# Performance work log

Hardware: AMD Instinct MI355X
Metric: run time of the kernel (lower is better)

Reference implementation:

```python
import jax, jax.numpy as jnp
import numpy as np

TOP_K = 12
OBS_RADIUS = 1.0
DIST_MIN_THRES = 0.8
EPS = 1e-4


def setup_inputs() -> dict:
    key = jax.random.key(0)
    ks = jax.random.split(key, 9)
    N, in_dim = 4096, 4
    c = in_dim + 2  # pairwise diff + eye flag + (dist - thres)
    states = jax.random.normal(ks[0], (N, in_dim), dtype=jnp.float32) * 2.0
    def w(k, o, i):
        return jax.random.normal(k, (o, i), dtype=jnp.float32) * (1.0 / np.sqrt(i))
    return {
        "states": states,
        "W1": w(ks[1], 64, c),  "b1": jnp.zeros((64,), jnp.float32),
        "W2": w(ks[2], 128, 64), "b2": jnp.zeros((128,), jnp.float32),
        "W3": w(ks[3], 64, 128), "b3": jnp.zeros((64,), jnp.float32),
        "W4": w(ks[4], 1, 64),   "b4": jnp.zeros((1,), jnp.float32),
    }


def _conv1x1(h, W, b):
    # h: [N, C_in, L]; 1x1 Conv1d == channel matmul
    return jnp.einsum('oi,nil->nol', W, h) + b[None, :, None]


def reference(states, W1, b1, W2, b2, W3, b3, W4, b4):
    N = states.shape[0]
    # pairwise differences: [N, N, in_dim]
    x = states[:, None, :] - states[None, :, :]
    d_norm = jnp.sqrt(jnp.sum(jnp.square(x[:, :, :2]) + EPS, axis=2))  # [N, N]
    eye = jnp.eye(N, dtype=x.dtype)
    x = jnp.concatenate(
        [x, eye[:, :, None], (d_norm - DIST_MIN_THRES)[:, :, None]], axis=2
    )  # [N, N, c]
    # remove_distant_agents: keep TOP_K nearest neighbors per agent
    dn = jnp.sqrt(jnp.sum(jnp.square(x[:, :, :2]) + EPS, axis=2))  # [N, N]
    _, idx = jax.lax.top_k(-dn, TOP_K)                              # [N, k]
    x = jnp.take_along_axis(x, idx[:, :, None], axis=1)            # [N, k, c]
    dist = jnp.sqrt(jnp.sum(jnp.square(x[:, :, :2]) + EPS, axis=2, keepdims=True))  # [N,k,1]
    k, c = x.shape[1], x.shape[2]
    mask = (dist <= OBS_RADIUS).astype(x.dtype).reshape(-1, 1, k)  # [N,1,k] (reshape, as in source)
    h = x.reshape(-1, c, k)  # faithful: source uses reshape, NOT transpose
    h = jax.nn.relu(_conv1x1(h, W1, b1))
    h = jax.nn.relu(_conv1x1(h, W2, b2))
    h = jax.nn.relu(_conv1x1(h, W3, b3))
    h = _conv1x1(h, W4, b4)  # [N, 1, k]
    h = h * mask
    return h, mask
```

## Files before the change

kernel.cpp:

```cpp
#include <hip/hip_runtime.h>
#include <stdint.h>

#define NAG 4096
#define TOPK 12
#define EPSF 1e-4f
#define NT 256
#define PT (NAG / NT)
#define MTOT (NAG * TOPK)

typedef unsigned long long u64;
typedef short short8v __attribute__((ext_vector_type(8)));
typedef float f32x4 __attribute__((ext_vector_type(4)));

__device__ __forceinline__ u64 umin64(u64 a, u64 b) { return a < b ? a : b; }

__device__ __forceinline__ unsigned short f2bf(float f) {
    union { float f; unsigned u; } v; v.f = f;
    unsigned r = v.u + 0x7FFFu + ((v.u >> 16) & 1u);
    return (unsigned short)(r >> 16);
}

template <int CTRL>
__device__ __forceinline__ void dpp_min_step(unsigned &hi, unsigned &lo) {
    unsigned ohi = (unsigned)__builtin_amdgcn_update_dpp((int)hi, (int)hi, CTRL, 0xf, 0xf, false);
    unsigned olo = (unsigned)__builtin_amdgcn_update_dpp((int)lo, (int)lo, CTRL, 0xf, 0xf, false);
    bool t = (ohi < hi) || (ohi == hi && olo < lo);
    hi = t ? ohi : hi;
    lo = t ? olo : lo;
}

__global__ __launch_bounds__(NT, 8)
void cbf_select(const float* __restrict__ states,
                float* __restrict__ xbuf,
                float* __restrict__ out)
{
    const int i = blockIdx.x;
    const int t = threadIdx.x;
    const int lane = t & 63;
    const int wv = t >> 6;

    __shared__ float s_dn[NT * 17];
    __shared__ u64 s_min[NT];
    __shared__ int s_sel[TOPK];
    __shared__ float s_x[72];

    const float2* st2 = reinterpret_cast<const float2*>(states);
    const float si0 = states[i * 4 + 0];
    const float si1 = states[i * 4 + 1];

    float mind = 1e30f;
    int minu = 0;
#pragma unroll
    for (int u = 0; u < PT; ++u) {
        int j = u * NT + t;
        float2 sj = st2[j * 2];
        float dx0 = __fsub_rn(si0, sj.x);
        float dx1 = __fsub_rn(si1, sj.y);
        float d2 = __fadd_rn(__fadd_rn(__fmul_rn(dx0, dx0), EPSF),
                             __fadd_rn(__fmul_rn(dx1, dx1), EPSF));
        float dn = __fsqrt_rn(d2);
        s_dn[t * 17 + u] = dn;
        if (dn < mind) { mind = dn; minu = u; }
    }
    s_min[t] = ((u64)__float_as_uint(mind) << 32) | (unsigned)(minu * NT + t);
    __syncthreads();

    if (wv == 0) {
        unsigned khi[4], klo[4];
#pragma unroll
        for (int q = 0; q < 4; ++q) {
            u64 kk = s_min[lane + q * 64];
            klo[q] = (unsigned)(kk & 0xffffffffull);
            khi[q] = (unsigned)(kk >> 32);
        }
        for (int r = 0; r < TOPK; ++r) {
            unsigned hi = khi[0], lo = klo[0];
#pragma unroll
            for (int q = 1; q < 4; ++q) {
                bool tk = (khi[q] < hi) || (khi[q] == hi && klo[q] < lo);
                hi = tk ? khi[q] : hi;
                lo = tk ? klo[q] : lo;
            }
            dpp_min_step<0xB1>(hi, lo);
            dpp_min_step<0x4E>(hi, lo);
            dpp_min_step<0x124>(hi, lo);
            dpp_min_step<0x128>(hi, lo);
            dpp_min_step<0x142>(hi, lo);
            dpp_min_step<0x143>(hi, lo);
            int j = __builtin_amdgcn_readlane((int)lo, 63);
            int gp = j & (NT - 1);
            int uw = j >> 8;
            if (lane == 0) {
                s_sel[r] = j;
                s_dn[gp * 17 + uw] = 1e30f;
            }
            u64 kv[16];
#pragma unroll
            for (int u = 0; u < 16; ++u) {
                float d = s_dn[gp * 17 + u];
                d = (u == uw) ? 1e30f : d;
                kv[u] = ((u64)__float_as_uint(d) << 4) | (unsigned)u;
            }
#pragma unroll
            for (int st = 8; st > 0; st >>= 1)
#pragma unroll
                for (int q = 0; q < 8; ++q)
                    if (q < st) kv[q] = umin64(kv[q], kv[q + st]);
            unsigned numin = (unsigned)(kv[0] & 15ull);
            unsigned nhi = (unsigned)(kv[0] >> 4);
            unsigned nlo = numin * NT + (unsigned)gp;
            bool own = (gp & 63) == lane;
            int idx = gp >> 6;
#pragma unroll
            for (int q = 0; q < 4; ++q) {
                bool w = own && (idx == q);
                khi[q] = w ? nhi : khi[q];
                klo[q] = w ? nlo : klo[q];
            }
        }
    }
    __syncthreads();

    if (t < TOPK) {
        int j = s_sel[t];
        const float4 sj = reinterpret_cast<const float4*>(states)[j];
        const float4 si = reinterpret_cast<const float4*>(states)[i];
        float dx0 = __fsub_rn(si.x, sj.x);
        float dx1 = __fsub_rn(si.y, sj.y);
        float dx2 = __fsub_rn(si.z, sj.z);
        float dx3 = __fsub_rn(si.w, sj.w);
        float d2 = __fadd_rn(__fadd_rn(__fmul_rn(dx0, dx0), EPSF),
                             __fadd_rn(__fmul_rn(dx1, dx1), EPSF));
        float dn = __fsqrt_rn(d2);
        s_x[t * 6 + 0] = dx0;
        s_x[t * 6 + 1] = dx1;
        s_x[t * 6 + 2] = dx2;
        s_x[t * 6 + 3] = dx3;
        s_x[t * 6 + 4] = (j == i) ? 1.0f : 0.0f;
        s_x[t * 6 + 5] = __fsub_rn(dn, 0.8f);
        out[MTOT + i * TOPK + t] = (dn <= 1.0f) ? 1.0f : 0.0f;
    }
    __syncthreads();

    if (t < TOPK) {
        int m = i * TOPK + t;
        float4 v0 = {s_x[0 * 12 + t], s_x[1 * 12 + t], s_x[2 * 12 + t], s_x[3 * 12 + t]};
        float4 v1 = {s_x[4 * 12 + t], s_x[5 * 12 + t], 0.0f, 0.0f};
        reinterpret_cast<float4*>(xbuf + m * 8)[0] = v0;
        reinterpret_cast<float4*>(xbuf + m * 8)[1] = v1;
    }
}

__global__ __launch_bounds__(256)
void cbf_mlp(const float* __restrict__ xbuf,
             const float* __restrict__ W1, const float* __restrict__ b1,
             const float* __restrict__ W2, const float* __restrict__ b2,
             const float* __restrict__ W3, const float* __restrict__ b3,
             const float* __restrict__ W4, const float* __restrict__ b4,
             float* __restrict__ out)
{
    const int t = threadIdx.x;
    const int lane = t & 63;
    const int wv = t >> 6;
    const int r16 = lane & 15;
    const int hi = lane >> 4;
    const int m0 = blockIdx.x * 64 + wv * 16;

    __shared__ __align__(16) unsigned char s_h1[4 * 2048];
    __shared__ __align__(16) unsigned char s_h2[4 * 4096];
    unsigned char* lp1 = s_h1 + wv * 2048;
    unsigned char* lp2 = s_h2 + wv * 4096;

    const int mrow = m0 + r16;
    const float4 xa = reinterpret_cast<const float4*>(xbuf + mrow * 8)[0];
    const float4 xb = reinterpret_cast<const float4*>(xbuf + mrow * 8)[1];
    const float xc[6] = {xa.x, xa.y, xa.z, xa.w, xb.x, xb.y};

    unsigned short h1b[16];
#pragma unroll
    for (int ol = 0; ol < 16; ++ol) {
        int o = hi * 16 + ol;
        const float2* wr = reinterpret_cast<const float2*>(W1 + o * 6);
        float2 w0 = wr[0], w1 = wr[1], w2 = wr[2];
        float acc = b1[o];
        acc = fmaf(w0.x, xc[0], acc);
        acc = fmaf(w0.y, xc[1], acc);
        acc = fmaf(w1.x, xc[2], acc);
        acc = fmaf(w1.y, xc[3], acc);
        acc = fmaf(w2.x, xc[4], acc);
        acc = fmaf(w2.y, xc[5], acc);
        h1b[ol] = f2bf(fmaxf(acc, 0.0f));
    }
    {
        short8v p0, p1;
#pragma unroll
        for (int e = 0; e < 8; ++e) { p0[e] = (short)h1b[e]; p1[e] = (short)h1b[8 + e]; }
        int rowb = r16 * 128;
        *(short8v*)(lp1 + rowb + (((2 * hi + 0) ^ (r16 & 7)) * 16)) = p0;
        *(short8v*)(lp1 + rowb + (((2 * hi + 1) ^ (r16 & 7)) * 16)) = p1;
    }
    __syncthreads();

    short8v a0 = *(short8v*)(lp1 + r16 * 128 + (((0 + hi) ^ (r16 & 7)) * 16));
    short8v a1 = *(short8v*)(lp1 + r16 * 128 + (((4 + hi) ^ (r16 & 7)) * 16));
    const int c = r16;
#pragma unroll
    for (int nt = 0; nt < 8; ++nt) {
        const float* wrow = W2 + (nt * 16 + c) * 64;
        float4 g0 = *(const float4*)(wrow + 8 * hi);
        float4 g1 = *(const float4*)(wrow + 8 * hi + 4);
        float4 g2 = *(const float4*)(wrow + 32 + 8 * hi);
        float4 g3 = *(const float4*)(wrow + 36 + 8 * hi);
        short8v bf0, bf1;
        bf0[0] = (short)f2bf(g0.x); bf0[1] = (short)f2bf(g0.y);
        bf0[2] = (short)f2bf(g0.z); bf0[3] = (short)f2bf(g0.w);
        bf0[4] = (short)f2bf(g1.x); bf0[5] = (short)f2bf(g1.y);
        bf0[6] = (short)f2bf(g1.z); bf0[7] = (short)f2bf(g1.w);
        bf1[0] = (short)f2bf(g2.x); bf1[1] = (short)f2bf(g2.y);
        bf1[2] = (short)f2bf(g2.z); bf1[3] = (short)f2bf(g2.w);
        bf1[4] = (short)f2bf(g3.x); bf1[5] = (short)f2bf(g3.y);
        bf1[6] = (short)f2bf(g3.z); bf1[7] = (short)f2bf(g3.w);
        float bb = b2[nt * 16 + c];
        f32x4 acc = {bb, bb, bb, bb};
        acc = __builtin_amdgcn_mfma_f32_16x16x32_bf16(a0, bf0, acc, 0, 0, 0);
        acc = __builtin_amdgcn_mfma_f32_16x16x32_bf16(a1, bf1, acc, 0, 0, 0);
#pragma unroll
        for (int e = 0; e < 4; ++e) {
            unsigned short hv = f2bf(fmaxf(acc[e], 0.0f));
            int mr = 4 * hi + e;
            int slot = (2 * nt + (c >> 3)) ^ (mr & 15);
            *(unsigned short*)(lp2 + mr * 256 + slot * 16 + ((2 * c) & 15)) = hv;
        }
    }
    __syncthreads();

    short8v a3[4];
#pragma unroll
    for (int ks = 0; ks < 4; ++ks)
        a3[ks] = *(short8v*)(lp2 + r16 * 256 + (((4 * ks + hi) ^ r16) * 16));
    float h3r[4][4];
#pragma unroll
    for (int nt = 0; nt < 4; ++nt) {
        const float* wrow = W3 + (nt * 16 + c) * 128;
        float bb = b3[nt * 16 + c];
        f32x4 ac = {bb, bb, bb, bb};
#pragma unroll
        for (int ks = 0; ks < 4; ++ks) {
            float4 q0 = *(const float4*)(wrow + ks * 32 + 8 * hi);
            float4 q1 = *(const float4*)(wrow + ks * 32 + 8 * hi + 4);
            short8v bf;
            bf[0] = (short)f2bf(q0.x); bf[1] = (short)f2bf(q0.y);
            bf[2] = (short)f2bf(q0.z); bf[3] = (short)f2bf(q0.w);
            bf[4] = (short)f2bf(q1.x); bf[5] = (short)f2bf(q1.y);
            bf[6] = (short)f2bf(q1.z); bf[7] = (short)f2bf(q1.w);
            ac = __builtin_amdgcn_mfma_f32_16x16x32_bf16(a3[ks], bf, ac, 0, 0, 0);
        }
#pragma unroll
        for (int e = 0; e < 4; ++e) h3r[nt][e] = fmaxf(ac[e], 0.0f);
    }

    float w4c[4];
#pragma unroll
    for (int nt = 0; nt < 4; ++nt) w4c[nt] = W4[nt * 16 + c];
    float part[4];
#pragma unroll
    for (int e = 0; e < 4; ++e) {
        float p = h3r[0][e] * w4c[0];
        p = fmaf(h3r[1][e], w4c[1], p);
        p = fmaf(h3r[2][e], w4c[2], p);
        p = fmaf(h3r[3][e], w4c[3], p);
        part[e] = p;
    }
#pragma unroll
    for (int off = 1; off <= 8; off <<= 1) {
#pragma unroll
        for (int e = 0; e < 4; ++e)
            part[e] += __shfl_xor(part[e], off, 64);
    }
    if (c == 0) {
        float bb4 = b4[0];
#pragma unroll
        for (int e = 0; e < 4; ++e) {
            int m = m0 + 4 * hi + e;
            float mk = out[MTOT + m];
            out[m] = (part[e] + bb4) * mk;
        }
    }
}

extern "C" void kernel_launch(void* const* d_in, const int* in_sizes, int n_in,
                              void* d_out, int out_size, void* d_ws, size_t ws_size,
                              hipStream_t stream) {
    const float* states = (const float*)d_in[0];
    const float* W1 = (const float*)d_in[1];
    const float* b1 = (const float*)d_in[2];
    const float* W2 = (const float*)d_in[3];
    const float* b2 = (const float*)d_in[4];
    const float* W3 = (const float*)d_in[5];
    const float* b3 = (const float*)d_in[6];
    const float* W4 = (const float*)d_in[7];
    const float* b4 = (const float*)d_in[8];
    float* out = (float*)d_out;
    float* xbuf = (float*)d_ws;

    cbf_select<<<dim3(NAG), dim3(NT), 0, stream>>>(states, xbuf, out);
    cbf_mlp<<<dim3(MTOT / 64), dim3(256), 0, stream>>>(xbuf, W1, b1, W2, b2,
                                                       W3, b3, W4, b4, out);
}
```

Baseline: 124.1 us.

## Replace iterative top-k refill with threshold filter and rank-based selection

Each round of the wave-0 top-k loop no longer reloads a winner thread's 16 distances from shared memory to refill its candidate. Instead, the 12th smallest of the per-thread minima is used as a distance threshold. Every thread then appends its register-held distances at or below that threshold to a shared survivor list through an atomic counter, and one wave ranks the survivors by pairwise comparison to pick the top 12. This removes the large s_dn shared array and the serial shared-memory dependency chain inside the selection loop. In exchange it adds shared-memory atomics and an extra barrier, and the survivor list is capped at 128, so clustered inputs could drop true neighbours.

```diff
diff --git a/kernel.cpp b/kernel.cpp
--- a/kernel.cpp
+++ b/kernel.cpp
@@ -39,15 +39,20 @@
     const int lane = t & 63;
     const int wv = t >> 6;
 
-    __shared__ float s_dn[NT * 17];
     __shared__ u64 s_min[NT];
+    __shared__ u64 s_surv[128];
     __shared__ int s_sel[TOPK];
     __shared__ float s_x[72];
+    __shared__ unsigned s_cnt;
+    __shared__ unsigned s_T;
+
+    if (t == 0) s_cnt = 0;
 
     const float2* st2 = reinterpret_cast<const float2*>(states);
     const float si0 = states[i * 4 + 0];
     const float si1 = states[i * 4 + 1];
 
+    unsigned dnb[PT];
     float mind = 1e30f;
     int minu = 0;
 #pragma unroll
@@ -59,7 +64,7 @@
         float d2 = __fadd_rn(__fadd_rn(__fmul_rn(dx0, dx0), EPSF),
                              __fadd_rn(__fmul_rn(dx1, dx1), EPSF));
         float dn = __fsqrt_rn(d2);
-        s_dn[t * 17 + u] = dn;
+        dnb[u] = __float_as_uint(dn);
         if (dn < mind) { mind = dn; minu = u; }
     }
     s_min[t] = ((u64)__float_as_uint(mind) << 32) | (unsigned)(minu * NT + t);
@@ -73,6 +78,7 @@
             klo[q] = (unsigned)(kk & 0xffffffffull);
             khi[q] = (unsigned)(kk >> 32);
         }
+        unsigned Tb = 0;
         for (int r = 0; r < TOPK; ++r) {
             unsigned hi = khi[0], lo = klo[0];
 #pragma unroll
@@ -87,37 +93,45 @@
             dpp_min_step<0x128>(hi, lo);
             dpp_min_step<0x142>(hi, lo);
             dpp_min_step<0x143>(hi, lo);
-            int j = __builtin_amdgcn_readlane((int)lo, 63);
-            int gp = j & (NT - 1);
-            int uw = j >> 8;
-            if (lane == 0) {
-                s_sel[r] = j;
-                s_dn[gp * 17 + uw] = 1e30f;
+            unsigned hw = (unsigned)__builtin_amdgcn_readlane((int)hi, 63);
+            unsigned lw = (unsigned)__builtin_amdgcn_readlane((int)lo, 63);
+            Tb = hw;
+#pragma unroll
+            for (int q = 0; q < 4; ++q) {
+                bool w = (khi[q] == hw) && (klo[q] == lw);
+                khi[q] = w ? 0xFFFFFFFFu : khi[q];
             }
-            u64 kv[16];
-#pragma unroll
-            for (int u = 0; u < 16; ++u) {
-                float d = s_dn[gp * 17 + u];
-                d = (u == uw) ? 1e30f : d;
-                kv[u] = ((u64)__float_as_uint(d) << 4) | (unsigned)u;
+        }
+        if (lane == 0) s_T = Tb;
+    }
+    __syncthreads();
+
+    {
+        unsigned Tb = s_T;
+#pragma unroll
+        for (int u = 0; u < PT; ++u) {
+            if (dnb[u] <= Tb) {
+                unsigned slot = atomicAdd(&s_cnt, 1u);
+                if (slot < 128)
+                    s_surv[slot] = ((u64)dnb[u] << 32) | (unsigned)(u * NT + t);
             }
-#pragma unroll
-            for (int st = 8; st > 0; st >>= 1)
-#pragma unroll
-                for (int q = 0; q < 8; ++q)
-                    if (q < st) kv[q] = umin64(kv[q], kv[q + st]);
-            unsigned numin = (unsigned)(kv[0] & 15ull);
-            unsigned nhi = (unsigned)(kv[0] >> 4);
-            unsigned nlo = numin * NT + (unsigned)gp;
-            bool own = (gp & 63) == lane;
-            int idx = gp >> 6;
-#pragma unroll
-            for (int q = 0; q < 4; ++q) {
-                bool w = own && (idx == q);
-                khi[q] = w ? nhi : khi[q];
-                klo[q] = w ? nlo : klo[q];
-            }
-        }
+        }
+    }
+    __syncthreads();
+
+    if (wv == 0) {
+        int cnt = (int)s_cnt;
+        if (cnt > 128) cnt = 128;
+        u64 kA = (lane < cnt) ? s_surv[lane] : ~0ull;
+        u64 kB = (lane + 64 < cnt) ? s_surv[lane + 64] : ~0ull;
+        int rA = 0, rB = 0;
+        for (int q = 0; q < cnt; ++q) {
+            u64 kq = s_surv[q];
+            rA += (kq < kA) ? 1 : 0;
+            rB += (kq < kB) ? 1 : 0;
+        }
+        if (lane < cnt && rA < TOPK) s_sel[rA] = (int)(unsigned)(kA & 0xffffffffull);
+        if (lane + 64 < cnt && rB < TOPK) s_sel[rB] = (int)(unsigned)(kB & 0xffffffffull);
     }
     __syncthreads();
 
```

New measurement: 115.3 us. 1.08x faster.
